# Optimization experiments

Measured on AMD Instinct MI355X. Metric: run time of the kernel, lower is better.

Reference implementation:

```python
import jax, jax.numpy as jnp
import numpy as np

B, H, S, D = 2, 16, 2048, 64

def setup_inputs() -> dict:
    key = jax.random.key(0)
    kq, kk, kv, km = jax.random.split(key, 4)
    q = jax.random.normal(kq, (B, H, S, D), dtype=jnp.float32)
    k = jax.random.normal(kk, (B, H, S, D), dtype=jnp.float32)
    v = jax.random.normal(kv, (B, H, S, D), dtype=jnp.float32)
    mask = jax.random.randint(km, (B, 1, S, S), 0, 2, dtype=jnp.int32)
    return {"q": q, "k": k, "v": v, "mask": mask}

def reference(q, k, v, mask):
    d_model = q.shape[-1]
    # scores: [B, H, S, S]
    score = jnp.einsum('bhqd,bhkd->bhqk', q, k) / jnp.sqrt(jnp.float32(d_model))
    score = jnp.where(mask == 0, jnp.float32(-1e9), score)
    attn = jax.nn.softmax(score, axis=-1)
    return jnp.einsum('bhqk,bhkd->bhqd', attn, v)
```

## Files before the change

kernel.cpp:

```cpp
#include <hip/hip_runtime.h>
#include <hip/hip_bf16.h>


#define B_ 2
#define H_ 16
#define S_ 2048
#define D_ 64
#define BQ 64
#define BK 64
#define NT (S_ / BK)
#define PADW 72
#define TILEB (BK * D_ * 2)

typedef __attribute__((ext_vector_type(4))) float f32x4;
typedef __attribute__((ext_vector_type(8))) short bf16x8;
typedef __attribute__((ext_vector_type(4))) short bf16x4;

#define QSCALE 0.1803368801111137f
#define MASKNEG (-1.4426950408889634e9f)
#define RTH 8.0f

static __device__ __forceinline__ short f2bf(float f) {
  __hip_bfloat16 h = __float2bfloat16(f);
  short s; __builtin_memcpy(&s, &h, sizeof(s)); return s;
}
static __device__ __forceinline__ float fexp2(float x) {
  return __builtin_amdgcn_exp2f(x);
}
static __device__ __forceinline__ void gload_lds16(const void* g, void* l) {
  __builtin_amdgcn_global_load_lds(
      (__attribute__((address_space(1))) void*)g,
      (__attribute__((address_space(3))) void*)l, 16, 0, 0);
}

__global__ __launch_bounds__(256)
void pack_kv(const float* __restrict__ kg, const float* __restrict__ vg,
             short* __restrict__ kw, short* __restrict__ vw) {
  const int t   = blockIdx.x;
  const int bh  = blockIdx.y;
  const int tid = threadIdx.x;
  const float* kt = kg + ((size_t)bh * S_ + t * BK) * D_;
  const float* vt = vg + ((size_t)bh * S_ + t * BK) * D_;
  short* ko = kw + ((size_t)bh * NT + t) * (BK * D_);
  short* vo = vw + ((size_t)bh * NT + t) * (BK * D_);

  const int row = tid >> 2;
  const int swz = (row & 7) << 4;

  #pragma unroll
  for (int c = 0; c < 2; ++c) {
    const int x = (tid & 3) * 32 + c * 16;
    const int dsrc = (x ^ swz) >> 1;
    const float4 u0 = *(const float4*)(kt + row * D_ + dsrc);
    const float4 u1 = *(const float4*)(kt + row * D_ + dsrc + 4);
    bf16x8 w;
    w[0]=f2bf(u0.x); w[1]=f2bf(u0.y); w[2]=f2bf(u0.z); w[3]=f2bf(u0.w);
    w[4]=f2bf(u1.x); w[5]=f2bf(u1.y); w[6]=f2bf(u1.z); w[7]=f2bf(u1.w);
    *(bf16x8*)(ko + row * D_ + (x >> 1)) = w;
  }

  __shared__ float sv[BK][D_ + 1];
  #pragma unroll
  for (int i = 0; i < 4; ++i) {
    const int id = tid + 256 * i;
    const int r = id >> 4, c4 = (id & 15) * 4;
    const float4 u = *(const float4*)(vt + r * D_ + c4);
    sv[r][c4] = u.x; sv[r][c4+1] = u.y; sv[r][c4+2] = u.z; sv[r][c4+3] = u.w;
  }
  __syncthreads();
  #pragma unroll
  for (int c = 0; c < 2; ++c) {
    const int x = (tid & 3) * 32 + c * 16;
    const int ksrc = (x ^ swz) >> 1;
    bf16x8 w;
    #pragma unroll
    for (int j = 0; j < 8; ++j) w[j] = f2bf(sv[ksrc + j][row]);
    *(bf16x8*)(vo + row * D_ + (x >> 1)) = w;
  }
}

__global__ __launch_bounds__(256)
void pack_mask(const int* __restrict__ mg, unsigned long long* __restrict__ mw) {
  const int row  = blockIdx.x * 4 + (threadIdx.x >> 6);
  const int lane = threadIdx.x & 63;
  const int* mr = mg + (size_t)row * S_;
  unsigned long long* out = mw + (size_t)row * NT;
  for (int s = 0; s < NT; ++s) {
    const int v = mr[s * 64 + lane];
    const unsigned long long bal = __ballot(v != 0);
    if (lane == 0) out[s] = bal;
  }
}

__global__ __launch_bounds__(256, 4)
void attn_main(const float* __restrict__ qg, const short* __restrict__ kw,
               const short* __restrict__ vw,
               const unsigned long long* __restrict__ mw,
               float* __restrict__ outg) {
  __shared__ short sK[BK * D_];
  __shared__ short sVT[D_ * BK];
  __shared__ short sP[4][16][PADW];

  const int tid  = threadIdx.x;
  const int lane = tid & 63;
  const int wv   = tid >> 6;
  const int l15  = lane & 15;
  const int quad = lane >> 4;

  const int f  = blockIdx.y * 32 + blockIdx.x;
  const int nf = (f & 7) * 128 + (f >> 3);
  const int bh = nf >> 5;
  const int b  = bh >> 4;
  const int q0 = (nf & 31) * BQ;
  const int qw = q0 + wv * 16 + l15;

  bf16x8 qf[2];
  {
    const float* qrow = qg + ((size_t)bh * S_ + qw) * D_;
    #pragma unroll
    for (int ks = 0; ks < 2; ++ks) {
      const float4 u0 = *(const float4*)(qrow + ks*32 + quad*8);
      const float4 u1 = *(const float4*)(qrow + ks*32 + quad*8 + 4);
      bf16x8 fq;
      fq[0]=f2bf(u0.x*QSCALE); fq[1]=f2bf(u0.y*QSCALE);
      fq[2]=f2bf(u0.z*QSCALE); fq[3]=f2bf(u0.w*QSCALE);
      fq[4]=f2bf(u1.x*QSCALE); fq[5]=f2bf(u1.y*QSCALE);
      fq[6]=f2bf(u1.z*QSCALE); fq[7]=f2bf(u1.w*QSCALE);
      qf[ks] = fq;
    }
  }

  f32x4 O[4];
  #pragma unroll
  for (int dt = 0; dt < 4; ++dt) O[dt] = (f32x4){0.f, 0.f, 0.f, 0.f};
  float m = -3.0e38f, l = 0.f;

  const char* kt = (const char*)(kw + (size_t)bh * NT * BK * D_);
  const char* vt = (const char*)(vw + (size_t)bh * NT * BK * D_);
  const unsigned long long* mb = mw + ((size_t)b * S_ + qw) * NT;
  const int so = tid * 16;

  const int swz = (l15 & 7) << 4;
  const char* kb0 = (const char*)sK  + l15*128 + (( 0 + quad*16) ^ swz);
  const char* kb1 = (const char*)sK  + l15*128 + ((64 + quad*16) ^ swz);
  const char* vb0 = (const char*)sVT + l15*128 + (( 0 + quad*16) ^ swz);
  const char* vb1 = (const char*)sVT + l15*128 + ((64 + quad*16) ^ swz);

  for (int t = 0; t < NT; ++t) {
    __syncthreads();
    gload_lds16(kt + so,        (char*)sK  + so);
    gload_lds16(kt + 4096 + so, (char*)sK  + 4096 + so);
    gload_lds16(vt + so,        (char*)sVT + so);
    gload_lds16(vt + 4096 + so, (char*)sVT + 4096 + so);
    kt += TILEB; vt += TILEB;
    const unsigned long long m64 = mb[t];
    __syncthreads();

    f32x4 st[4];
    #pragma unroll
    for (int mt = 0; mt < 4; ++mt) {
      f32x4 acc = (f32x4){0.f, 0.f, 0.f, 0.f};
      const bf16x8 kf0 = *(const bf16x8*)(kb0 + mt*2048);
      const bf16x8 kf1 = *(const bf16x8*)(kb1 + mt*2048);
      acc = __builtin_amdgcn_mfma_f32_16x16x32_bf16(kf0, qf[0], acc, 0, 0, 0);
      acc = __builtin_amdgcn_mfma_f32_16x16x32_bf16(kf1, qf[1], acc, 0, 0, 0);
      st[mt] = acc;
    }

    float cmax = -3.0e38f;
    #pragma unroll
    for (int mt = 0; mt < 4; ++mt) {
      cmax = fmaxf(cmax, fmaxf(fmaxf(st[mt].x, st[mt].y),
                               fmaxf(st[mt].z, st[mt].w)));
    }
    cmax = fmaxf(cmax, __shfl_xor(cmax, 16));
    cmax = fmaxf(cmax, __shfl_xor(cmax, 32));

    if (!__all(cmax - m <= RTH)) {
      const float mnew  = fmaxf(m, cmax);
      const float alpha = fexp2(m - mnew);
      m = mnew;
      l *= alpha;
      const float ar0 = __shfl(alpha, quad*4 + 0);
      const float ar1 = __shfl(alpha, quad*4 + 1);
      const float ar2 = __shfl(alpha, quad*4 + 2);
      const float ar3 = __shfl(alpha, quad*4 + 3);
      #pragma unroll
      for (int dt = 0; dt < 4; ++dt) {
        O[dt].x *= ar0; O[dt].y *= ar1; O[dt].z *= ar2; O[dt].w *= ar3;
      }
    }

    const unsigned lo = (unsigned)(m64 >> (quad * 4));
    const unsigned hi = (unsigned)(m64 >> (quad * 4 + 32));
    float lsum = 0.f;
    #pragma unroll
    for (int mt = 0; mt < 4; ++mt) {
      const unsigned w32 = (mt < 2) ? lo : hi;
      const int bb = (mt & 1) * 16;
      float p0 = fexp2(st[mt].x - m);
      float p1 = fexp2(st[mt].y - m);
      float p2 = fexp2(st[mt].z - m);
      float p3 = fexp2(st[mt].w - m);
      p0 = __uint_as_float(__float_as_uint(p0) &
             (unsigned)((int)(w32 << (31 - (bb + 0))) >> 31));
      p1 = __uint_as_float(__float_as_uint(p1) &
             (unsigned)((int)(w32 << (31 - (bb + 1))) >> 31));
      p2 = __uint_as_float(__float_as_uint(p2) &
             (unsigned)((int)(w32 << (31 - (bb + 2))) >> 31));
      p3 = __uint_as_float(__float_as_uint(p3) &
             (unsigned)((int)(w32 << (31 - (bb + 3))) >> 31));
      lsum += (p0 + p1) + (p2 + p3);
      bf16x4 pw; pw[0]=f2bf(p0); pw[1]=f2bf(p1); pw[2]=f2bf(p2); pw[3]=f2bf(p3);
      *(bf16x4*)&sP[wv][l15][mt*16 + quad*4] = pw;
    }
    lsum += __shfl_xor(lsum, 16);
    lsum += __shfl_xor(lsum, 32);
    l += lsum;

    asm volatile("s_waitcnt lgkmcnt(0)" ::: "memory");

    const bf16x8 pf0 = *(const bf16x8*)&sP[wv][l15][quad*8];
    const bf16x8 pf1 = *(const bf16x8*)&sP[wv][l15][32 + quad*8];
    #pragma unroll
    for (int dt = 0; dt < 4; ++dt) {
      const bf16x8 vf0 = *(const bf16x8*)(vb0 + dt*2048);
      const bf16x8 vf1 = *(const bf16x8*)(vb1 + dt*2048);
      O[dt] = __builtin_amdgcn_mfma_f32_16x16x32_bf16(pf0, vf0, O[dt], 0, 0, 0);
      O[dt] = __builtin_amdgcn_mfma_f32_16x16x32_bf16(pf1, vf1, O[dt], 0, 0, 0);
    }
  }

  float ir[4];
  #pragma unroll
  for (int r = 0; r < 4; ++r) ir[r] = 1.0f / __shfl(l, quad*4 + r);

  float* ob = outg + ((size_t)bh * S_ + q0 + wv*16) * D_;
  #pragma unroll
  for (int dt = 0; dt < 4; ++dt) {
    ob[(quad*4 + 0)*D_ + dt*16 + l15] = O[dt].x * ir[0];
    ob[(quad*4 + 1)*D_ + dt*16 + l15] = O[dt].y * ir[1];
    ob[(quad*4 + 2)*D_ + dt*16 + l15] = O[dt].z * ir[2];
    ob[(quad*4 + 3)*D_ + dt*16 + l15] = O[dt].w * ir[3];
  }
}

__global__ __launch_bounds__(256, 4)
void attn_fallback(const float* __restrict__ qg, const float* __restrict__ kg,
                   const float* __restrict__ vg, const int* __restrict__ maskg,
                   float* __restrict__ outg) {
  __shared__ short sK[BK][PADW];
  __shared__ short sVT[D_][PADW];
  __shared__ short sP[4][16][PADW];

  const int tid  = threadIdx.x;
  const int lane = tid & 63;
  const int wv   = tid >> 6;
  const int l15  = lane & 15;
  const int quad = lane >> 4;

  const int bh = blockIdx.y;
  const int b  = bh >> 4;
  const int q0 = blockIdx.x * BQ;
  const int qw = q0 + wv * 16 + l15;

  bf16x8 qf[2];
  {
    const float* qrow = qg + ((size_t)bh * S_ + qw) * D_;
    #pragma unroll
    for (int ks = 0; ks < 2; ++ks) {
      const float4 u0 = *(const float4*)(qrow + ks*32 + quad*8);
      const float4 u1 = *(const float4*)(qrow + ks*32 + quad*8 + 4);
      bf16x8 fq;
      fq[0]=f2bf(u0.x*QSCALE); fq[1]=f2bf(u0.y*QSCALE);
      fq[2]=f2bf(u0.z*QSCALE); fq[3]=f2bf(u0.w*QSCALE);
      fq[4]=f2bf(u1.x*QSCALE); fq[5]=f2bf(u1.y*QSCALE);
      fq[6]=f2bf(u1.z*QSCALE); fq[7]=f2bf(u1.w*QSCALE);
      qf[ks] = fq;
    }
  }

  f32x4 O[4];
  #pragma unroll
  for (int dt = 0; dt < 4; ++dt) O[dt] = (f32x4){0.f, 0.f, 0.f, 0.f};
  float m = -3.0e38f, l = 0.f;

  const float* kbase = kg + (size_t)bh * S_ * D_;
  const float* vbase = vg + (size_t)bh * S_ * D_;
  const int*   mrow  = maskg + ((size_t)b * S_ + qw) * S_;

  for (int t0 = 0; t0 < S_; t0 += BK) {
    __syncthreads();
    #pragma unroll
    for (int i = 0; i < 4; ++i) {
      const int id = tid + 256*i;
      const int key = id >> 4, d4 = (id & 15) * 4;
      const float4 u = *(const float4*)(kbase + (size_t)(t0 + key)*D_ + d4);
      bf16x4 w; w[0]=f2bf(u.x); w[1]=f2bf(u.y); w[2]=f2bf(u.z); w[3]=f2bf(u.w);
      *(bf16x4*)&sK[key][d4] = w;
    }
    #pragma unroll
    for (int i = 0; i < 2; ++i) {
      const int id = tid + 256*i;
      const int kp = id & 31, d4 = (id >> 5) * 4;
      const float4 a = *(const float4*)(vbase + (size_t)(t0 + 2*kp    )*D_ + d4);
      const float4 c = *(const float4*)(vbase + (size_t)(t0 + 2*kp + 1)*D_ + d4);
      const float av[4] = {a.x, a.y, a.z, a.w};
      const float cv[4] = {c.x, c.y, c.z, c.w};
      #pragma unroll
      for (int j = 0; j < 4; ++j) {
        const unsigned pk = (unsigned)(unsigned short)f2bf(av[j])
                          | ((unsigned)(unsigned short)f2bf(cv[j]) << 16);
        *(unsigned*)&sVT[d4 + j][2*kp] = pk;
      }
    }
    __syncthreads();

    int4 mk[4];
    #pragma unroll
    for (int mt = 0; mt < 4; ++mt)
      mk[mt] = *(const int4*)(mrow + t0 + mt*16 + quad*4);

    f32x4 st[4];
    #pragma unroll
    for (int mt = 0; mt < 4; ++mt) {
      f32x4 acc = (f32x4){0.f, 0.f, 0.f, 0.f};
      #pragma unroll
      for (int ks = 0; ks < 2; ++ks) {
        const bf16x8 kf = *(const bf16x8*)&sK[mt*16 + l15][ks*32 + quad*8];
        acc = __builtin_amdgcn_mfma_f32_16x16x32_bf16(kf, qf[ks], acc, 0, 0, 0);
      }
      st[mt] = acc;
    }

    float cmax = -3.0e38f;
    #pragma unroll
    for (int mt = 0; mt < 4; ++mt) {
      f32x4 s = st[mt];
      s.x = mk[mt].x ? s.x : MASKNEG;
      s.y = mk[mt].y ? s.y : MASKNEG;
      s.z = mk[mt].z ? s.z : MASKNEG;
      s.w = mk[mt].w ? s.w : MASKNEG;
      st[mt] = s;
      cmax = fmaxf(cmax, fmaxf(fmaxf(s.x, s.y), fmaxf(s.z, s.w)));
    }
    cmax = fmaxf(cmax, __shfl_xor(cmax, 16));
    cmax = fmaxf(cmax, __shfl_xor(cmax, 32));
    const float mnew  = fmaxf(m, cmax);
    const float alpha = fexp2(m - mnew);
    m = mnew;

    float lsum = 0.f;
    #pragma unroll
    for (int mt = 0; mt < 4; ++mt) {
      const float p0 = fexp2(st[mt].x - mnew);
      const float p1 = fexp2(st[mt].y - mnew);
      const float p2 = fexp2(st[mt].z - mnew);
      const float p3 = fexp2(st[mt].w - mnew);
      lsum += (p0 + p1) + (p2 + p3);
      bf16x4 pw; pw[0]=f2bf(p0); pw[1]=f2bf(p1); pw[2]=f2bf(p2); pw[3]=f2bf(p3);
      *(bf16x4*)&sP[wv][l15][mt*16 + quad*4] = pw;
    }
    lsum += __shfl_xor(lsum, 16);
    lsum += __shfl_xor(lsum, 32);
    l = l * alpha + lsum;

    const float ar0 = __shfl(alpha, quad*4 + 0);
    const float ar1 = __shfl(alpha, quad*4 + 1);
    const float ar2 = __shfl(alpha, quad*4 + 2);
    const float ar3 = __shfl(alpha, quad*4 + 3);
    #pragma unroll
    for (int dt = 0; dt < 4; ++dt) {
      O[dt].x *= ar0; O[dt].y *= ar1; O[dt].z *= ar2; O[dt].w *= ar3;
    }

    asm volatile("s_waitcnt lgkmcnt(0)" ::: "memory");

    const bf16x8 pf0 = *(const bf16x8*)&sP[wv][l15][quad*8];
    const bf16x8 pf1 = *(const bf16x8*)&sP[wv][l15][32 + quad*8];
    #pragma unroll
    for (int dt = 0; dt < 4; ++dt) {
      const bf16x8 vf0 = *(const bf16x8*)&sVT[dt*16 + l15][quad*8];
      const bf16x8 vf1 = *(const bf16x8*)&sVT[dt*16 + l15][32 + quad*8];
      O[dt] = __builtin_amdgcn_mfma_f32_16x16x32_bf16(pf0, vf0, O[dt], 0, 0, 0);
      O[dt] = __builtin_amdgcn_mfma_f32_16x16x32_bf16(pf1, vf1, O[dt], 0, 0, 0);
    }
  }

  float ir[4];
  #pragma unroll
  for (int r = 0; r < 4; ++r) ir[r] = 1.0f / __shfl(l, quad*4 + r);

  float* ob = outg + ((size_t)bh * S_ + q0 + wv*16) * D_;
  #pragma unroll
  for (int dt = 0; dt < 4; ++dt) {
    ob[(quad*4 + 0)*D_ + dt*16 + l15] = O[dt].x * ir[0];
    ob[(quad*4 + 1)*D_ + dt*16 + l15] = O[dt].y * ir[1];
    ob[(quad*4 + 2)*D_ + dt*16 + l15] = O[dt].z * ir[2];
    ob[(quad*4 + 3)*D_ + dt*16 + l15] = O[dt].w * ir[3];
  }
}

extern "C" void kernel_launch(void* const* d_in, const int* in_sizes, int n_in,
                              void* d_out, int out_size, void* d_ws, size_t ws_size,
                              hipStream_t stream) {
  const float* q    = (const float*)d_in[0];
  const float* k    = (const float*)d_in[1];
  const float* v    = (const float*)d_in[2];
  const int*   mask = (const int*)d_in[3];
  float* out = (float*)d_out;

  const size_t kvbytes = (size_t)B_ * H_ * S_ * D_ * 2;
  const size_t mbytes  = (size_t)B_ * S_ * NT * 8;
  const size_t need    = 2 * kvbytes + mbytes;

  if (d_ws != nullptr && ws_size >= need) {
    short* kwp = (short*)d_ws;
    short* vwp = (short*)((char*)d_ws + kvbytes);
    unsigned long long* mwp = (unsigned long long*)((char*)d_ws + 2 * kvbytes);
    pack_kv<<<dim3(NT, B_ * H_), 256, 0, stream>>>(k, v, kwp, vwp);
    pack_mask<<<dim3(B_ * S_ / 4), 256, 0, stream>>>(mask, mwp);
    attn_main<<<dim3(S_ / BQ, B_ * H_), 256, 0, stream>>>(q, kwp, vwp, mwp, out);
  } else {
    attn_fallback<<<dim3(S_ / BQ, B_ * H_), 256, 0, stream>>>(q, k, v, mask, out);
  }
}
```

Measured before the change: 197.6 us.

## Double-buffer K/V tiles, widen query block to 128, fuse pack kernels

The attention kernel now processes 128 query rows per block with 8 waves, so each staged K/V tile is reused by twice as many queries. K/V tiles are double-buffered in LDS with asynchronous loads for the next tile issued before the current compute, using one barrier per iteration. MFMA sections are bracketed with s_setprio, bf16 conversion uses packed cvt instructions, and the P buffer is swizzled. The K/V and mask packing kernels are merged into one launch, with vectorised mask loads and a permuted bit layout. In exchange, LDS use per block rises and the grid shrinks to fewer, larger blocks, which may lower occupancy.

Measured after the change: 177.2 us. 1.11x faster.

```diff
diff --git a/kernel.cpp b/kernel.cpp
--- a/kernel.cpp
+++ b/kernel.cpp
@@ -6,7 +6,8 @@
 #define H_ 16
 #define S_ 2048
 #define D_ 64
-#define BQ 64
+#define BQ 128
+#define NW 8
 #define BK 64
 #define NT (S_ / BK)
 #define PADW 72
@@ -27,6 +28,11 @@
 static __device__ __forceinline__ float fexp2(float x) {
   return __builtin_amdgcn_exp2f(x);
 }
+static __device__ __forceinline__ unsigned cvt_pk_bf16(float a, float b) {
+  unsigned r;
+  asm("v_cvt_pk_bf16_f32 %0, %1, %2" : "=v"(r) : "v"(a), "v"(b));
+  return r;
+}
 static __device__ __forceinline__ void gload_lds16(const void* g, void* l) {
   __builtin_amdgcn_global_load_lds(
       (__attribute__((address_space(1))) void*)g,
@@ -34,72 +40,90 @@
 }
 
 __global__ __launch_bounds__(256)
-void pack_kv(const float* __restrict__ kg, const float* __restrict__ vg,
-             short* __restrict__ kw, short* __restrict__ vw) {
-  const int t   = blockIdx.x;
-  const int bh  = blockIdx.y;
+void pack_all(const float* __restrict__ kg, const float* __restrict__ vg,
+              const int* __restrict__ mg,
+              short* __restrict__ kw, short* __restrict__ vw,
+              unsigned long long* __restrict__ mwp) {
+  __shared__ float sv[BK][D_ + 1];
+  const int bx  = blockIdx.x;
   const int tid = threadIdx.x;
-  const float* kt = kg + ((size_t)bh * S_ + t * BK) * D_;
-  const float* vt = vg + ((size_t)bh * S_ + t * BK) * D_;
-  short* ko = kw + ((size_t)bh * NT + t) * (BK * D_);
-  short* vo = vw + ((size_t)bh * NT + t) * (BK * D_);
-
-  const int row = tid >> 2;
-  const int swz = (row & 7) << 4;
-
-  #pragma unroll
-  for (int c = 0; c < 2; ++c) {
-    const int x = (tid & 3) * 32 + c * 16;
-    const int dsrc = (x ^ swz) >> 1;
-    const float4 u0 = *(const float4*)(kt + row * D_ + dsrc);
-    const float4 u1 = *(const float4*)(kt + row * D_ + dsrc + 4);
-    bf16x8 w;
-    w[0]=f2bf(u0.x); w[1]=f2bf(u0.y); w[2]=f2bf(u0.z); w[3]=f2bf(u0.w);
-    w[4]=f2bf(u1.x); w[5]=f2bf(u1.y); w[6]=f2bf(u1.z); w[7]=f2bf(u1.w);
-    *(bf16x8*)(ko + row * D_ + (x >> 1)) = w;
-  }
-
-  __shared__ float sv[BK][D_ + 1];
-  #pragma unroll
-  for (int i = 0; i < 4; ++i) {
-    const int id = tid + 256 * i;
-    const int r = id >> 4, c4 = (id & 15) * 4;
-    const float4 u = *(const float4*)(vt + r * D_ + c4);
-    sv[r][c4] = u.x; sv[r][c4+1] = u.y; sv[r][c4+2] = u.z; sv[r][c4+3] = u.w;
-  }
-  __syncthreads();
-  #pragma unroll
-  for (int c = 0; c < 2; ++c) {
-    const int x = (tid & 3) * 32 + c * 16;
-    const int ksrc = (x ^ swz) >> 1;
-    bf16x8 w;
-    #pragma unroll
-    for (int j = 0; j < 8; ++j) w[j] = f2bf(sv[ksrc + j][row]);
-    *(bf16x8*)(vo + row * D_ + (x >> 1)) = w;
-  }
-}
-
-__global__ __launch_bounds__(256)
-void pack_mask(const int* __restrict__ mg, unsigned long long* __restrict__ mw) {
-  const int row  = blockIdx.x * 4 + (threadIdx.x >> 6);
-  const int lane = threadIdx.x & 63;
-  const int* mr = mg + (size_t)row * S_;
-  unsigned long long* out = mw + (size_t)row * NT;
-  for (int s = 0; s < NT; ++s) {
-    const int v = mr[s * 64 + lane];
-    const unsigned long long bal = __ballot(v != 0);
-    if (lane == 0) out[s] = bal;
-  }
-}
-
-__global__ __launch_bounds__(256, 4)
+
+  if (bx < 1024) {
+    const int t  = bx & 31;
+    const int bh = bx >> 5;
+    const float* kt = kg + ((size_t)bh * S_ + t * BK) * D_;
+    const float* vt = vg + ((size_t)bh * S_ + t * BK) * D_;
+    short* ko = kw + ((size_t)bh * NT + t) * (BK * D_);
+    short* vo = vw + ((size_t)bh * NT + t) * (BK * D_);
+
+    const int row = tid >> 2;
+    const int swz = (row & 7) << 4;
+
+    #pragma unroll
+    for (int c = 0; c < 2; ++c) {
+      const int x = (tid & 3) * 32 + c * 16;
+      const int dsrc = (x ^ swz) >> 1;
+      const float4 u0 = *(const float4*)(kt + row * D_ + dsrc);
+      const float4 u1 = *(const float4*)(kt + row * D_ + dsrc + 4);
+      uint4 w;
+      w.x = cvt_pk_bf16(u0.x, u0.y); w.y = cvt_pk_bf16(u0.z, u0.w);
+      w.z = cvt_pk_bf16(u1.x, u1.y); w.w = cvt_pk_bf16(u1.z, u1.w);
+      *(uint4*)(ko + row * D_ + (x >> 1)) = w;
+    }
+
+    #pragma unroll
+    for (int i = 0; i < 4; ++i) {
+      const int id = tid + 256 * i;
+      const int r = id >> 4, c4 = (id & 15) * 4;
+      const float4 u = *(const float4*)(vt + r * D_ + c4);
+      sv[r][c4] = u.x; sv[r][c4+1] = u.y; sv[r][c4+2] = u.z; sv[r][c4+3] = u.w;
+    }
+    __syncthreads();
+    #pragma unroll
+    for (int c = 0; c < 2; ++c) {
+      const int x = (tid & 3) * 32 + c * 16;
+      const int ksrc = (x ^ swz) >> 1;
+      uint4 w;
+      w.x = cvt_pk_bf16(sv[ksrc+0][row], sv[ksrc+1][row]);
+      w.y = cvt_pk_bf16(sv[ksrc+2][row], sv[ksrc+3][row]);
+      w.z = cvt_pk_bf16(sv[ksrc+4][row], sv[ksrc+5][row]);
+      w.w = cvt_pk_bf16(sv[ksrc+6][row], sv[ksrc+7][row]);
+      *(uint4*)(vo + row * D_ + (x >> 1)) = w;
+    }
+  } else {
+    const int r4   = bx - 1024;
+    const int wv   = tid >> 6;
+    const int lane = tid & 63;
+    const int row  = r4 * 4 + wv;
+    const int* mr = mg + (size_t)row * S_;
+    unsigned long long* out = mwp + (size_t)row * NT;
+    #pragma unroll
+    for (int g = 0; g < 8; ++g) {
+      const int4 v = *(const int4*)(mr + g * 256 + lane * 4);
+      const unsigned long long b0 = __ballot(v.x != 0);
+      const unsigned long long b1 = __ballot(v.y != 0);
+      const unsigned long long b2 = __ballot(v.z != 0);
+      const unsigned long long b3 = __ballot(v.w != 0);
+      if (lane < 4) {
+        const int tl = lane;
+        const unsigned long long u =
+            ((b0 >> (16 * tl)) & 0xFFFFULL)
+          | (((b1 >> (16 * tl)) & 0xFFFFULL) << 16)
+          | (((b2 >> (16 * tl)) & 0xFFFFULL) << 32)
+          | (((b3 >> (16 * tl)) & 0xFFFFULL) << 48);
+        out[g * 4 + tl] = u;
+      }
+    }
+  }
+}
+
+__global__ __launch_bounds__(512, 4)
 void attn_main(const float* __restrict__ qg, const short* __restrict__ kw,
                const short* __restrict__ vw,
                const unsigned long long* __restrict__ mw,
                float* __restrict__ outg) {
-  __shared__ short sK[BK * D_];
-  __shared__ short sVT[D_ * BK];
-  __shared__ short sP[4][16][PADW];
+  __shared__ short sKV[2][2][BK * D_];
+  __shared__ short sP[NW][16][64];
 
   const int tid  = threadIdx.x;
   const int lane = tid & 63;
@@ -107,11 +131,11 @@
   const int l15  = lane & 15;
   const int quad = lane >> 4;
 
-  const int f  = blockIdx.y * 32 + blockIdx.x;
-  const int nf = (f & 7) * 128 + (f >> 3);
-  const int bh = nf >> 5;
+  const int f  = blockIdx.y * 16 + blockIdx.x;
+  const int nf = (f & 7) * 64 + (f >> 3);
+  const int bh = nf >> 4;
   const int b  = bh >> 4;
-  const int q0 = (nf & 31) * BQ;
+  const int q0 = (nf & 15) * BQ;
   const int qw = q0 + wv * 16 + l15;
 
   bf16x8 qf[2];
@@ -141,38 +165,45 @@
   const int so = tid * 16;
 
   const int swz = (l15 & 7) << 4;
-  const char* kb0 = (const char*)sK  + l15*128 + (( 0 + quad*16) ^ swz);
-  const char* kb1 = (const char*)sK  + l15*128 + ((64 + quad*16) ^ swz);
-  const char* vb0 = (const char*)sVT + l15*128 + (( 0 + quad*16) ^ swz);
-  const char* vb1 = (const char*)sVT + l15*128 + ((64 + quad*16) ^ swz);
+  const int ro0 = l15*128 + (( 0 + quad*16) ^ swz);
+  const int ro1 = l15*128 + ((64 + quad*16) ^ swz);
+  char* const spw = (char*)sP + wv*2048;
+
+  gload_lds16(kt + so, (char*)sKV + so);
+  gload_lds16(vt + so, (char*)sKV + 8192 + so);
+  kt += TILEB; vt += TILEB;
+  int cur = 0;
+  __syncthreads();
 
   for (int t = 0; t < NT; ++t) {
-    __syncthreads();
-    gload_lds16(kt + so,        (char*)sK  + so);
-    gload_lds16(kt + 4096 + so, (char*)sK  + 4096 + so);
-    gload_lds16(vt + so,        (char*)sVT + so);
-    gload_lds16(vt + 4096 + so, (char*)sVT + 4096 + so);
-    kt += TILEB; vt += TILEB;
     const unsigned long long m64 = mb[t];
-    __syncthreads();
+    if (t < NT - 1) {
+      const int nb = (cur ^ 1) << 14;
+      gload_lds16(kt + so, (char*)sKV + nb + so);
+      gload_lds16(vt + so, (char*)sKV + nb + 8192 + so);
+      kt += TILEB; vt += TILEB;
+    }
+    const char* kb = (const char*)sKV + (cur << 14);
+    const char* vb = kb + 8192;
 
     f32x4 st[4];
+    __builtin_amdgcn_s_setprio(1);
     #pragma unroll
     for (int mt = 0; mt < 4; ++mt) {
       f32x4 acc = (f32x4){0.f, 0.f, 0.f, 0.f};
-      const bf16x8 kf0 = *(const bf16x8*)(kb0 + mt*2048);
-      const bf16x8 kf1 = *(const bf16x8*)(kb1 + mt*2048);
+      const bf16x8 kf0 = *(const bf16x8*)(kb + mt*2048 + ro0);
+      const bf16x8 kf1 = *(const bf16x8*)(kb + mt*2048 + ro1);
       acc = __builtin_amdgcn_mfma_f32_16x16x32_bf16(kf0, qf[0], acc, 0, 0, 0);
       acc = __builtin_amdgcn_mfma_f32_16x16x32_bf16(kf1, qf[1], acc, 0, 0, 0);
       st[mt] = acc;
     }
-
-    float cmax = -3.0e38f;
-    #pragma unroll
-    for (int mt = 0; mt < 4; ++mt) {
-      cmax = fmaxf(cmax, fmaxf(fmaxf(st[mt].x, st[mt].y),
-                               fmaxf(st[mt].z, st[mt].w)));
-    }
+    __builtin_amdgcn_s_setprio(0);
+
+    float c0 = fmaxf(fmaxf(st[0].x, st[0].y), fmaxf(st[0].z, st[0].w));
+    float c1 = fmaxf(fmaxf(st[1].x, st[1].y), fmaxf(st[1].z, st[1].w));
+    float c2 = fmaxf(fmaxf(st[2].x, st[2].y), fmaxf(st[2].z, st[2].w));
+    float c3 = fmaxf(fmaxf(st[3].x, st[3].y), fmaxf(st[3].z, st[3].w));
+    float cmax = fmaxf(fmaxf(c0, c1), fmaxf(c2, c3));
     cmax = fmaxf(cmax, __shfl_xor(cmax, 16));
     cmax = fmaxf(cmax, __shfl_xor(cmax, 32));
 
@@ -191,28 +222,28 @@
       }
     }
 
-    const unsigned lo = (unsigned)(m64 >> (quad * 4));
-    const unsigned hi = (unsigned)(m64 >> (quad * 4 + 32));
+    const unsigned xlo = ((unsigned)m64) >> quad;
+    const unsigned xhi = ((unsigned)(m64 >> 32)) >> quad;
     float lsum = 0.f;
     #pragma unroll
     for (int mt = 0; mt < 4; ++mt) {
-      const unsigned w32 = (mt < 2) ? lo : hi;
-      const int bb = (mt & 1) * 16;
       float p0 = fexp2(st[mt].x - m);
       float p1 = fexp2(st[mt].y - m);
       float p2 = fexp2(st[mt].z - m);
       float p3 = fexp2(st[mt].w - m);
-      p0 = __uint_as_float(__float_as_uint(p0) &
-             (unsigned)((int)(w32 << (31 - (bb + 0))) >> 31));
-      p1 = __uint_as_float(__float_as_uint(p1) &
-             (unsigned)((int)(w32 << (31 - (bb + 1))) >> 31));
-      p2 = __uint_as_float(__float_as_uint(p2) &
-             (unsigned)((int)(w32 << (31 - (bb + 2))) >> 31));
-      p3 = __uint_as_float(__float_as_uint(p3) &
-             (unsigned)((int)(w32 << (31 - (bb + 3))) >> 31));
+      const unsigned a0 = (unsigned)(((int)(xlo << (31 - mt*4))) >> 31);
+      const unsigned a1 = (unsigned)(((int)(xlo << (15 - mt*4))) >> 31);
+      const unsigned a2 = (unsigned)(((int)(xhi << (31 - mt*4))) >> 31);
+      const unsigned a3 = (unsigned)(((int)(xhi << (15 - mt*4))) >> 31);
+      p0 = __uint_as_float(__float_as_uint(p0) & a0);
+      p1 = __uint_as_float(__float_as_uint(p1) & a1);
+      p2 = __uint_as_float(__float_as_uint(p2) & a2);
+      p3 = __uint_as_float(__float_as_uint(p3) & a3);
       lsum += (p0 + p1) + (p2 + p3);
-      bf16x4 pw; pw[0]=f2bf(p0); pw[1]=f2bf(p1); pw[2]=f2bf(p2); pw[3]=f2bf(p3);
-      *(bf16x4*)&sP[wv][l15][mt*16 + quad*4] = pw;
+      uint2 uu;
+      uu.x = cvt_pk_bf16(p0, p1);
+      uu.y = cvt_pk_bf16(p2, p3);
+      *(uint2*)(spw + l15*128 + ((mt*32 + quad*8) ^ swz)) = uu;
     }
     lsum += __shfl_xor(lsum, 16);
     lsum += __shfl_xor(lsum, 32);
@@ -220,15 +251,20 @@
 
     asm volatile("s_waitcnt lgkmcnt(0)" ::: "memory");
 
-    const bf16x8 pf0 = *(const bf16x8*)&sP[wv][l15][quad*8];
-    const bf16x8 pf1 = *(const bf16x8*)&sP[wv][l15][32 + quad*8];
+    const bf16x8 pf0 = *(const bf16x8*)(spw + l15*128 + (( 0 + quad*16) ^ swz));
+    const bf16x8 pf1 = *(const bf16x8*)(spw + l15*128 + ((64 + quad*16) ^ swz));
+    __builtin_amdgcn_s_setprio(1);
     #pragma unroll
     for (int dt = 0; dt < 4; ++dt) {
-      const bf16x8 vf0 = *(const bf16x8*)(vb0 + dt*2048);
-      const bf16x8 vf1 = *(const bf16x8*)(vb1 + dt*2048);
+      const bf16x8 vf0 = *(const bf16x8*)(vb + dt*2048 + ro0);
+      const bf16x8 vf1 = *(const bf16x8*)(vb + dt*2048 + ro1);
       O[dt] = __builtin_amdgcn_mfma_f32_16x16x32_bf16(pf0, vf0, O[dt], 0, 0, 0);
       O[dt] = __builtin_amdgcn_mfma_f32_16x16x32_bf16(pf1, vf1, O[dt], 0, 0, 0);
     }
+    __builtin_amdgcn_s_setprio(0);
+
+    __syncthreads();
+    cur ^= 1;
   }
 
   float ir[4];
@@ -261,7 +297,7 @@
 
   const int bh = blockIdx.y;
   const int b  = bh >> 4;
-  const int q0 = blockIdx.x * BQ;
+  const int q0 = blockIdx.x * 64;
   const int qw = q0 + wv * 16 + l15;
 
   bf16x8 qf[2];
@@ -418,10 +454,9 @@
     short* kwp = (short*)d_ws;
     short* vwp = (short*)((char*)d_ws + kvbytes);
     unsigned long long* mwp = (unsigned long long*)((char*)d_ws + 2 * kvbytes);
-    pack_kv<<<dim3(NT, B_ * H_), 256, 0, stream>>>(k, v, kwp, vwp);
-    pack_mask<<<dim3(B_ * S_ / 4), 256, 0, stream>>>(mask, mwp);
-    attn_main<<<dim3(S_ / BQ, B_ * H_), 256, 0, stream>>>(q, kwp, vwp, mwp, out);
+    pack_all<<<dim3(2048), 256, 0, stream>>>(k, v, mask, kwp, vwp, mwp);
+    attn_main<<<dim3(S_ / BQ, B_ * H_), 512, 0, stream>>>(q, kwp, vwp, mwp, out);
   } else {
-    attn_fallback<<<dim3(S_ / BQ, B_ * H_), 256, 0, stream>>>(q, k, v, mask, out);
-  }
-}
+    attn_fallback<<<dim3(S_ / 64, B_ * H_), 256, 0, stream>>>(q, k, v, mask, out);
+  }
+}
```
